# Optimization experiments

Measured on AMD Instinct MI355X. Metric: run time of the kernel, lower is better.

The kernel has to match this reference:

```python
import jax, jax.numpy as jnp
import numpy as np

B, S, D = 2, 2048, 768
H, HD = 12, 64            # num_heads, head_dim
TOPO = 128                # topology_dim
NH, HB = 8, 64            # num_hashes, hash_bits
TEMP = 0.1                # lsh_temperature
SCALE = float(np.sqrt(HD))
LSH_THRESH = 0.3
NEG = -10000.0


def setup_inputs() -> dict:
    key = jax.random.key(0)
    ks = jax.random.split(key, 12)
    hidden_states = jax.random.normal(ks[0], (B, S, D), jnp.float32)
    topo_features = jax.random.normal(ks[1], (B, S, TOPO), jnp.float32)
    attention_mask = jnp.ones((B, S), jnp.int32)
    s = 0.02
    Wq = jax.random.normal(ks[2], (D, D), jnp.float32) * s
    Wk = jax.random.normal(ks[3], (D, D), jnp.float32) * s
    Wv = jax.random.normal(ks[4], (D, D), jnp.float32) * s
    Wo = jax.random.normal(ks[5], (D, D), jnp.float32) * s
    bo = jnp.zeros((D,), jnp.float32)
    Wg = jax.random.normal(ks[6], (D + TOPO, D), jnp.float32) * s
    bg = jnp.zeros((D,), jnp.float32)
    hash_proj = jax.random.normal(ks[7], (NH, D, HB), jnp.float32) * 0.02
    topology_bias = jnp.zeros((NH, HB), jnp.float32)
    return {
        "hidden_states": hidden_states, "topo_features": topo_features,
        "Wq": Wq, "Wk": Wk, "Wv": Wv, "Wo": Wo, "bo": bo,
        "Wg": Wg, "bg": bg, "hash_proj": hash_proj,
        "topology_bias": topology_bias, "attention_mask": attention_mask,
    }


def reference(hidden_states, topo_features, Wq, Wk, Wv, Wo, bo, Wg, bg,
              hash_proj, topology_bias, attention_mask):
    hs, tf = hidden_states, topo_features
    # QKV projections -> [B,H,S,HD]
    q = (hs @ Wq).reshape(B, S, H, HD).transpose(0, 2, 1, 3)
    k = (hs @ Wk).reshape(B, S, H, HD).transpose(0, 2, 1, 3)
    v = (hs @ Wv).reshape(B, S, H, HD).transpose(0, 2, 1, 3)
    scores = jnp.einsum('bhqd,bhkd->bhqk', q, k) / SCALE  # [B,H,S,S]

    # LSH hash codes (queries == keys == hidden_states)
    proj = jnp.einsum('bsd,hdk->bshk', hs, hash_proj)
    proj = proj + TEMP * jnp.einsum('bsd,hdk->bshk', tf, hash_proj[:, :TOPO, :])
    proj = proj + topology_bias[None, None]  # [B,S,NH,HB]
    codes = jnp.sign(proj)
    # hash similarity averaged over hash tables -> [B,S,S]
    sim = jnp.einsum('bqhc,bkhc->bhqk', codes, codes) / HB
    sim = sim.mean(axis=1)
    lsh_keep = sim > LSH_THRESH
    scores = jnp.where(lsh_keep[:, None], scores, NEG)

    pad_keep = (attention_mask != 0)[:, None, None, :]  # [B,1,1,S]
    scores = jnp.where(pad_keep, scores, NEG)

    probs = jax.nn.softmax(scores, axis=-1)
    context = jnp.einsum('bhqk,bhkd->bqhd', probs, v).reshape(B, S, D)

    gate = jax.nn.sigmoid(jnp.concatenate([context, tf], axis=-1) @ Wg + bg)
    context = gate * context + (1.0 - gate) * hs
    return context @ Wo + bo
```

## Files before the change

kernel.cpp:

```cpp
#include <hip/hip_runtime.h>

typedef __attribute__((ext_vector_type(4))) float v4f;
typedef __attribute__((ext_vector_type(8))) short v8s;

#define BB 2
#define SS 2048
#define DD 768
#define HH 12
#define HDIM 64
#define NWORDS 8
#define HAM_MAX 179

#define OFF_QBF    ((size_t)0)
#define OFF_HSBF   ((size_t)31457280)
#define OFF_TFBF   ((size_t)37748736)
#define OFF_CTXBF  ((size_t)38797312)
#define OFF_CTX2BF ((size_t)45088768)
#define OFF_WTQKV  ((size_t)51380224)
#define OFF_WGT    ((size_t)54919168)
#define OFF_WOT    ((size_t)56295424)
#define OFF_HPWT   ((size_t)57475072)
#define OFF_CODES  ((size_t)66781184)
#define OFF_KEEP   ((size_t)67043328)
#define OFF_CMASK  ((size_t)68091904)

__device__ inline short f2bf(float x) {
    unsigned u = __float_as_uint(x);
    u = (u + 0x7FFFu + ((u >> 16) & 1u)) >> 16;
    return (short)u;
}
__device__ inline float bf2f(short s) {
    return __uint_as_float(((unsigned)(unsigned short)s) << 16);
}

__device__ __forceinline__ void load_lds16(const void* g, void* l) {
    __builtin_amdgcn_global_load_lds((const __attribute__((address_space(1))) void*)g,
                                     (__attribute__((address_space(3))) void*)l,
                                     16, 0, 0);
}

__global__ __launch_bounds__(256) void prep(
    const float* __restrict__ hs, const float* __restrict__ tf,
    const float* __restrict__ Wq, const float* __restrict__ Wk,
    const float* __restrict__ Wv, const float* __restrict__ Wg,
    const float* __restrict__ Wo, const float* __restrict__ hp,
    short* __restrict__ hsbf, short* __restrict__ tfbf,
    short* __restrict__ wtqkv, short* __restrict__ wgT,
    short* __restrict__ woT, short* __restrict__ hpwT,
    unsigned int* __restrict__ cmask) {
    __shared__ float T[32][33];
    const int blk = blockIdx.x;
    const int tid = threadIdx.x;
    if (blk < 1792) {
        if (blk == 0 && tid < 64) cmask[tid] = 0u;
        int i = blk * 256 + tid;
        const int na8 = 3145728 / 8;
        const float* src; short* dst; int off;
        if (i < na8) { src = hs; dst = hsbf; off = i << 3; }
        else         { src = tf; dst = tfbf; off = (i - na8) << 3; }
        float4 x = *(const float4*)(src + off);
        float4 y = *(const float4*)(src + off + 4);
        v8s r;
        r[0] = f2bf(x.x); r[1] = f2bf(x.y); r[2] = f2bf(x.z); r[3] = f2bf(x.w);
        r[4] = f2bf(y.x); r[5] = f2bf(y.y); r[6] = f2bf(y.z); r[7] = f2bf(y.w);
        *(v8s*)(dst + off) = r;
        return;
    }
    const int tx = tid & 31, ty = tid >> 5;
    if (blk < 3520) {
        int b = blk - 1792;
        int z = b / 576, rem = b % 576;
        int x = rem % 24, y = rem / 24;
        const float* W = (z == 0) ? Wq : (z == 1) ? Wk : Wv;
        short* Wt = wtqkv + (size_t)z * 589824;
        int n0 = x * 32, k0 = y * 32;
#pragma unroll
        for (int p = 0; p < 4; ++p) {
            int kk = ty + p * 8;
            T[tx][kk] = W[(size_t)(k0 + kk) * 768 + n0 + tx];
        }
        __syncthreads();
#pragma unroll
        for (int p = 0; p < 4; ++p) {
            int nn = ty + p * 8;
            Wt[(size_t)(n0 + nn) * 768 + k0 + tx] = f2bf(T[nn][tx]);
        }
    } else if (blk < 4192) {
        int b = blk - 3520;
        int x = b % 24, y = b / 24;
        int n0 = x * 32, k0 = y * 32;
#pragma unroll
        for (int p = 0; p < 4; ++p) {
            int kk = ty + p * 8;
            T[tx][kk] = Wg[(size_t)(k0 + kk) * 768 + n0 + tx];
        }
        __syncthreads();
#pragma unroll
        for (int p = 0; p < 4; ++p) {
            int nn = ty + p * 8;
            wgT[(size_t)(n0 + nn) * 896 + k0 + tx] = f2bf(T[nn][tx]);
        }
    } else if (blk < 4768) {
        int b = blk - 4192;
        int x = b % 24, y = b / 24;
        int n0 = x * 32, k0 = y * 32;
#pragma unroll
        for (int p = 0; p < 4; ++p) {
            int kk = ty + p * 8;
            T[tx][kk] = Wo[(size_t)(k0 + kk) * 768 + n0 + tx];
        }
        __syncthreads();
#pragma unroll
        for (int p = 0; p < 4; ++p) {
            int nn = ty + p * 8;
            woT[(size_t)(n0 + nn) * 768 + k0 + tx] = f2bf(T[nn][tx]);
        }
    } else {
        int b = blk - 4768;
        int x = b % 28, y = b / 28;
        int kk0 = x * 32, hc0 = y * 32;
        int h = hc0 >> 6, cb = hc0 & 63;
#pragma unroll
        for (int p = 0; p < 4; ++p) {
            int kp = ty + p * 8;
            int gk = kk0 + kp;
            int ks = (gk >= 768) ? gk - 768 : gk;
            float f = hp[((size_t)h * 768 + ks) * 64 + cb + tx];
            T[tx][kp] = (gk >= 768) ? 0.1f * f : f;
        }
        __syncthreads();
#pragma unroll
        for (int p = 0; p < 4; ++p) {
            int cp = ty + p * 8;
            hpwT[(size_t)(hc0 + cp) * 896 + kk0 + tx] = f2bf(T[cp][tx]);
        }
    }
}

template<int WN, int NW>
__global__ __launch_bounds__(256) void gemm_mfma(
    const short* __restrict__ A, const short* __restrict__ A2,
    const short* __restrict__ Bt, const short* __restrict__ Bt2,
    const float* __restrict__ bias,
    float* __restrict__ outF, short* __restrict__ outB,
    unsigned long long* __restrict__ codesOut,
    int N, int K1, int K2, int mode,
    const short* __restrict__ gctxb, const short* __restrict__ ghsb) {
    constexpr int BN = WN * 32;
    __shared__ __align__(16) short As[2 * 128 * 64];
    __shared__ __align__(16) short Bs[2 * NW * BN * 64];
    const int t = threadIdx.x;
    const int lane = t & 63, wave = t >> 6;
    const int wm = wave >> 1, wn = wave & 1;
    const int l15 = lane & 15, l4 = lane >> 4;

    const int nbx = gridDim.x;
    int flat = blockIdx.x + nbx * blockIdx.y;
    int xcd = flat & 7, j = flat >> 3;
    int by = xcd * 4 + j / nbx;
    int bx = j % nbx;
    const int row0 = by * 128;

    int nWact, col0, myMode, Kblk;
    const short* Bp;
    const float* biasp = bias;
    if (mode == 3) {
        if (bx < 12) { nWact = NW; col0 = bx * 64;        myMode = 1; Kblk = K1;      Bp = Bt;  biasp = nullptr; }
        else         { nWact = 2;  col0 = (bx - 12) * 128; myMode = 0; Kblk = K1 + K2; Bp = Bt2; }
    } else {
        nWact = 1; col0 = bx * BN; myMode = mode; Kblk = K1 + K2; Bp = Bt;
    }
    const bool sepW = (myMode == 1);

    const int lrow = lane >> 3;
    const int scolS = ((lane & 7) ^ lrow) << 3;

    auto STAGE = [&](int buf, int k0) {
        const short* Ap; int ks, strideS;
        if (k0 < K1) { Ap = A;  ks = k0;      strideS = K1; }
        else         { Ap = A2; ks = k0 - K1; strideS = K2; }
#pragma unroll
        for (int qq = 0; qq < 4; ++qq) {
            int c = wave * 4 + qq;
            const short* ga = Ap + (size_t)(row0 + c * 8 + lrow) * strideS + ks + scolS;
            load_lds16(ga, (char*)As + buf * 16384 + c * 1024);
        }
#pragma unroll
        for (int w = 0; w < NW; ++w) {
            if (w < nWact) {
#pragma unroll
                for (int qq = 0; qq < WN; ++qq) {
                    int c = wave * WN + qq;
                    size_t rowIdx = (size_t)(col0 + (sepW ? 0 : w * 64) + c * 8 + lrow);
                    const short* gb = Bp + (sepW ? (size_t)w * 589824 : (size_t)0) +
                                      rowIdx * Kblk + k0 + scolS;
                    load_lds16(gb, (char*)Bs + (buf * NW + w) * (BN * 128) + c * 1024);
                }
            }
        }
    };

    v4f acc[NW][4][WN];
#pragma unroll
    for (int w = 0; w < NW; ++w)
#pragma unroll
        for (int m = 0; m < 4; ++m)
#pragma unroll
            for (int n = 0; n < WN; ++n) acc[w][m][n] = (v4f){0.f, 0.f, 0.f, 0.f};

    const int nK = Kblk >> 6;
    STAGE(0, 0);
    __syncthreads();
    int cur = 0;
    for (int kt = 0; kt < nK; ++kt) {
        if (kt + 1 < nK) STAGE(cur ^ 1, (kt + 1) << 6);
#pragma unroll
        for (int kk = 0; kk < 2; ++kk) {
            v8s a[4];
#pragma unroll
            for (int m = 0; m < 4; ++m) {
                int row = wm * 64 + m * 16 + l15;
                int byte = (row * 128 + kk * 64 + l4 * 16) ^ ((row & 7) << 4);
                a[m] = *(const v8s*)((const char*)As + cur * 16384 + byte);
            }
#pragma unroll
            for (int w = 0; w < NW; ++w) {
                if (w < nWact) {
                    v8s b[WN];
#pragma unroll
                    for (int n = 0; n < WN; ++n) {
                        int row = wn * (WN * 16) + n * 16 + l15;
                        int byte = (row * 128 + kk * 64 + l4 * 16) ^ ((row & 7) << 4);
                        b[n] = *(const v8s*)((const char*)Bs + (cur * NW + w) * (BN * 128) + byte);
                    }
#pragma unroll
                    for (int m = 0; m < 4; ++m)
#pragma unroll
                        for (int n = 0; n < WN; ++n)
                            acc[w][m][n] = __builtin_amdgcn_mfma_f32_16x16x32_bf16(a[m], b[n], acc[w][m][n], 0, 0, 0);
                }
            }
        }
        __syncthreads();
        cur ^= 1;
    }

    if (mode == 3 && myMode == 0) {
        unsigned short* pieces = (unsigned short*)As;
#pragma unroll
        for (int w = 0; w < 2; ++w)
#pragma unroll
            for (int m = 0; m < 4; ++m)
#pragma unroll
                for (int n = 0; n < WN; ++n) {
                    int gc = col0 + w * 64 + (wn * WN + n) * 16 + l15;
                    int part = w * 4 + wn * WN + n;
#pragma unroll
                    for (int i = 0; i < 4; ++i) {
                        float c = acc[w][m][n][i] + biasp[gc];
                        unsigned long long bal = __ballot(c > 0.f);
                        if (lane < 4) {
                            int rloc = wm * 64 + m * 16 + lane * 4 + i;
                            pieces[rloc * 8 + part] = (unsigned short)(bal >> (lane * 16));
                        }
                    }
                }
        __syncthreads();
        if (t < 256) {
            int row = t >> 1, word = t & 1;
            const unsigned short* pp = pieces + row * 8 + word * 4;
            unsigned long long w64 = (unsigned long long)pp[0]
                | ((unsigned long long)pp[1] << 16)
                | ((unsigned long long)pp[2] << 32)
                | ((unsigned long long)pp[3] << 48);
            codesOut[(size_t)(row0 + row) * NWORDS + ((col0 >> 6) + word)] = w64;
        }
        return;
    }

#pragma unroll
    for (int m = 0; m < 4; ++m) {
#pragma unroll
        for (int n = 0; n < WN; ++n) {
            int gr0 = row0 + (wm * 4 + m) * 16 + l4 * 4;
            int gc = col0 + (wn * WN + n) * 16 + l15;
#pragma unroll
            for (int i = 0; i < 4; ++i) {
                int gr = gr0 + i;
                if (myMode == 1) {
                    int bb = gr >> 11, s = gr & 2047;
                    int h = gc >> 6, hd = gc & 63;
                    size_t base = (((size_t)(bb * HH + h)) * SS + s) * HDIM + hd;
#pragma unroll
                    for (int w = 0; w < NW; ++w)
                        if (w < nWact)
                            outB[(size_t)w * 3145728 + base] = f2bf(acc[w][m][n][i]);
                } else if (myMode == 0) {
                    float c = acc[0][m][n][i];
                    if (biasp) c += biasp[gc];
                    outF[(size_t)gr * N + gc] = c;
                } else {
                    float c = acc[0][m][n][i] + biasp[gc];
                    float g = 1.f / (1.f + __expf(-c));
                    size_t off = (size_t)gr * N + gc;
                    float cv = bf2f(gctxb[off]);
                    float hv = bf2f(ghsb[off]);
                    outB[off] = f2bf(g * cv + (1.f - g) * hv);
                }
            }
        }
    }
}

__global__ __launch_bounds__(256) void mask_kernel(
    const unsigned long long* __restrict__ codes, const int* __restrict__ mask,
    unsigned long long* __restrict__ keepArr, unsigned int* __restrict__ chunkmask) {
    __shared__ unsigned long long ckS[64][NWORDS];
    __shared__ int mskS[64];
    const int t = threadIdx.x;
    const int r = t >> 2, tx = t & 3;
    const int qc = blockIdx.x, kc = blockIdx.y, b = blockIdx.z;
    const int q0 = qc << 6, k0 = kc << 6;

#pragma unroll
    for (int p = 0; p < 2; ++p) {
        int idx = t + (p << 8);
        int jr = idx >> 3, ww = idx & 7;
        ckS[jr][ww ^ (jr >> 4)] =
            codes[((size_t)(b * SS + k0 + jr)) * NWORDS + ww];
    }
    if (t < 64) mskS[t] = mask[b * SS + k0 + t];
    unsigned long long cq[NWORDS];
    {
        const unsigned long long* cp = codes + ((size_t)(b * SS + q0 + r)) * NWORDS;
#pragma unroll
        for (int w = 0; w < NWORDS; ++w) cq[w] = cp[w];
    }
    __syncthreads();

    unsigned long long k64 = 0;
#pragma unroll
    for (int j16 = 0; j16 < 16; ++j16) {
        int j = (tx << 4) + j16;
        int ham = 0;
#pragma unroll
        for (int w = 0; w < NWORDS; ++w)
            ham += __popcll(cq[w] ^ ckS[j][w ^ tx]);
        if (ham <= HAM_MAX && mskS[j]) k64 |= 1ull << j;
    }
    k64 |= __shfl_xor(k64, 1, 4);
    k64 |= __shfl_xor(k64, 2, 4);
    if (tx == 0) keepArr[((size_t)(b * SS + q0 + r)) * 32 + kc] = k64;
    if (__syncthreads_or(k64 != 0) && t == 0)
        atomicOr(&chunkmask[b * 32 + qc], 1u << kc);
}

__global__ __launch_bounds__(256) void attn_kernel(
    const short* __restrict__ qm, const short* __restrict__ km,
    const short* __restrict__ vm, const unsigned long long* __restrict__ keepArr,
    const unsigned int* __restrict__ chunkmask, short* __restrict__ ctxbf) {
    __shared__ __align__(16) short Qs[64][72];
    __shared__ __align__(16) short Ks[64][72];
    __shared__ __align__(16) short VT[64][72];
    __shared__ __align__(16) short Ps[64][72];
    __shared__ unsigned long long keepS[64];
    const int t = threadIdx.x;
    const int lane = t & 63, wave = t >> 6;
    const int l15 = lane & 15, l4 = lane >> 4;
    const int q0 = blockIdx.x << 6;
    const int bh = blockIdx.y;
    const int b = bh / HH, h = bh % HH;

    {
        int r = t >> 2, seg = t & 3;
        const short* g = qm + ((size_t)bh * SS + q0 + r) * HDIM + seg * 16;
        *(int4*)&Qs[r][seg * 16] = *(const int4*)g;
        *(int4*)&Qs[r][seg * 16 + 8] = *(const int4*)(g + 8);
    }
    unsigned int cm = chunkmask[b * 32 + blockIdx.x];
    float mrun[4], lrun[4];
    v4f oacc[4];
#pragma unroll
    for (int i = 0; i < 4; ++i) { mrun[i] = -1e30f; lrun[i] = 0.f; }
#pragma unroll
    for (int n = 0; n < 4; ++n) oacc[n] = (v4f){0.f, 0.f, 0.f, 0.f};

    while (cm) {
        int kc = __ffs(cm) - 1;
        cm &= cm - 1;
        __syncthreads();
        if (t < 64) keepS[t] = keepArr[((size_t)(b * SS + q0 + t)) * 32 + kc];
        {
            int key = t >> 2, seg = t & 3;
            const short* gk = km + ((size_t)bh * SS + (kc << 6) + key) * HDIM + seg * 16;
            *(int4*)&Ks[key][seg * 16] = *(const int4*)gk;
            *(int4*)&Ks[key][seg * 16 + 8] = *(const int4*)(gk + 8);
            const short* gv = vm + ((size_t)bh * SS + (kc << 6) + key) * HDIM + seg * 16;
            int4 v0 = *(const int4*)gv, v1 = *(const int4*)(gv + 8);
            const short* s0 = (const short*)&v0;
            const short* s1 = (const short*)&v1;
#pragma unroll
            for (int e = 0; e < 8; ++e) VT[seg * 16 + e][key] = s0[e];
#pragma unroll
            for (int e = 0; e < 8; ++e) VT[seg * 16 + 8 + e][key] = s1[e];
        }
        __syncthreads();

        v8s qa0 = *(const v8s*)&Qs[wave * 16 + l15][l4 * 8];
        v8s qa1 = *(const v8s*)&Qs[wave * 16 + l15][32 + l4 * 8];
        v4f sacc[4];
#pragma unroll
        for (int n = 0; n < 4; ++n) sacc[n] = (v4f){0.f, 0.f, 0.f, 0.f};
#pragma unroll
        for (int n = 0; n < 4; ++n) {
            v8s kb0 = *(const v8s*)&Ks[n * 16 + l15][l4 * 8];
            v8s kb1 = *(const v8s*)&Ks[n * 16 + l15][32 + l4 * 8];
            sacc[n] = __builtin_amdgcn_mfma_f32_16x16x32_bf16(qa0, kb0, sacc[n], 0, 0, 0);
            sacc[n] = __builtin_amdgcn_mfma_f32_16x16x32_bf16(qa1, kb1, sacc[n], 0, 0, 0);
        }
        unsigned long long kp[4];
#pragma unroll
        for (int i = 0; i < 4; ++i) kp[i] = keepS[wave * 16 + l4 * 4 + i];
        float pe[4][4], mloc[4];
#pragma unroll
        for (int i = 0; i < 4; ++i) mloc[i] = -1e30f;
#pragma unroll
        for (int n = 0; n < 4; ++n)
#pragma unroll
            for (int i = 0; i < 4; ++i) {
                bool keep = (kp[i] >> (n * 16 + l15)) & 1;
                float sv = keep ? sacc[n][i] * 0.125f : -1e30f;
                pe[n][i] = sv;
                mloc[i] = fmaxf(mloc[i], sv);
            }
#pragma unroll
        for (int i = 0; i < 4; ++i) {
            mloc[i] = fmaxf(mloc[i], __shfl_xor(mloc[i], 1, 16));
            mloc[i] = fmaxf(mloc[i], __shfl_xor(mloc[i], 2, 16));
            mloc[i] = fmaxf(mloc[i], __shfl_xor(mloc[i], 4, 16));
            mloc[i] = fmaxf(mloc[i], __shfl_xor(mloc[i], 8, 16));
        }
        float psum[4] = {0.f, 0.f, 0.f, 0.f};
#pragma unroll
        for (int n = 0; n < 4; ++n)
#pragma unroll
            for (int i = 0; i < 4; ++i) {
                bool keep = pe[n][i] > -1e29f;
                float mnew = fmaxf(mrun[i], mloc[i]);
                float p = keep ? __expf(pe[n][i] - mnew) : 0.f;
                pe[n][i] = p;
                psum[i] += p;
            }
#pragma unroll
        for (int i = 0; i < 4; ++i) {
            psum[i] += __shfl_xor(psum[i], 1, 16);
            psum[i] += __shfl_xor(psum[i], 2, 16);
            psum[i] += __shfl_xor(psum[i], 4, 16);
            psum[i] += __shfl_xor(psum[i], 8, 16);
            float mnew = fmaxf(mrun[i], mloc[i]);
            float scale = __expf(mrun[i] - mnew);
            lrun[i] = lrun[i] * scale + psum[i];
            mrun[i] = mnew;
#pragma unroll
            for (int n = 0; n < 4; ++n) oacc[n][i] *= scale;
        }
#pragma unroll
        for (int n = 0; n < 4; ++n)
#pragma unroll
            for (int i = 0; i < 4; ++i)
                Ps[wave * 16 + l4 * 4 + i][n * 16 + l15] = f2bf(pe[n][i]);
        __syncthreads();

        v8s pa0 = *(const v8s*)&Ps[wave * 16 + l15][l4 * 8];
        v8s pa1 = *(const v8s*)&Ps[wave * 16 + l15][32 + l4 * 8];
#pragma unroll
        for (int n = 0; n < 4; ++n) {
            v8s vb0 = *(const v8s*)&VT[n * 16 + l15][l4 * 8];
            v8s vb1 = *(const v8s*)&VT[n * 16 + l15][32 + l4 * 8];
            oacc[n] = __builtin_amdgcn_mfma_f32_16x16x32_bf16(pa0, vb0, oacc[n], 0, 0, 0);
            oacc[n] = __builtin_amdgcn_mfma_f32_16x16x32_bf16(pa1, vb1, oacc[n], 0, 0, 0);
        }
    }
    float invl[4];
#pragma unroll
    for (int i = 0; i < 4; ++i) invl[i] = lrun[i] > 0.f ? 1.f / lrun[i] : 0.f;
#pragma unroll
    for (int n = 0; n < 4; ++n)
#pragma unroll
        for (int i = 0; i < 4; ++i) {
            int r = wave * 16 + l4 * 4 + i;
            size_t off = ((size_t)b * SS + q0 + r) * DD + h * HDIM + n * 16 + l15;
            ctxbf[off] = f2bf(oacc[n][i] * invl[i]);
        }
}

extern "C" void kernel_launch(void* const* d_in, const int* in_sizes, int n_in,
                              void* d_out, int out_size, void* d_ws, size_t ws_size,
                              hipStream_t stream) {
    const float* hs = (const float*)d_in[0];
    const float* tf = (const float*)d_in[1];
    const float* Wq = (const float*)d_in[2];
    const float* Wk = (const float*)d_in[3];
    const float* Wv = (const float*)d_in[4];
    const float* Wo = (const float*)d_in[5];
    const float* bo = (const float*)d_in[6];
    const float* Wg = (const float*)d_in[7];
    const float* bg = (const float*)d_in[8];
    const float* hp = (const float*)d_in[9];
    const float* tb = (const float*)d_in[10];
    const int* msk  = (const int*)d_in[11];
    float* out = (float*)d_out;

    char* w = (char*)d_ws;
    short* qkvbf  = (short*)(w + OFF_QBF);
    short* hsbf   = (short*)(w + OFF_HSBF);
    short* tfbf   = (short*)(w + OFF_TFBF);
    short* ctxbf  = (short*)(w + OFF_CTXBF);
    short* ctx2bf = (short*)(w + OFF_CTX2BF);
    short* wtqkv  = (short*)(w + OFF_WTQKV);
    short* wgT    = (short*)(w + OFF_WGT);
    short* woT    = (short*)(w + OFF_WOT);
    short* hpwT   = (short*)(w + OFF_HPWT);
    unsigned long long* codes = (unsigned long long*)(w + OFF_CODES);
    unsigned long long* keepA = (unsigned long long*)(w + OFF_KEEP);
    unsigned int* cmask = (unsigned int*)(w + OFF_CMASK);

    prep<<<dim3(5216), 256, 0, stream>>>(
        hs, tf, Wq, Wk, Wv, Wg, Wo, hp,
        hsbf, tfbf, wtqkv, wgT, woT, hpwT, cmask);
    gemm_mfma<2, 3><<<dim3(16, 32), 256, 0, stream>>>(
        hsbf, tfbf, wtqkv, hpwT, tb, nullptr, qkvbf, codes,
        512, 768, 128, 3, nullptr, nullptr);
    mask_kernel<<<dim3(32, 32, 2), 256, 0, stream>>>(codes, msk, keepA, cmask);
    attn_kernel<<<dim3(32, 24), 256, 0, stream>>>(
        qkvbf, qkvbf + 3145728, qkvbf + 2 * 3145728, keepA, cmask, ctxbf);
    gemm_mfma<2, 1><<<dim3(12, 32), 256, 0, stream>>>(
        ctxbf, tfbf, wgT, nullptr, bg, nullptr, ctx2bf, nullptr,
        768, 768, 128, 2, ctxbf, hsbf);
    gemm_mfma<2, 1><<<dim3(12, 32), 256, 0, stream>>>(
        ctx2bf, nullptr, woT, nullptr, bo, out, nullptr, nullptr,
        768, 768, 0, 0, nullptr, nullptr);
}
```

Before: 104.0 us.

## Parameterize GEMM M-tile, halve tiles for gate/output GEMMs, stage QKV stores via LDS

Adds an MF template parameter so the GEMM row-tile height (BM) is configurable. The gate and output-projection GEMMs now use 64-row tiles with twice as many blocks, to fill more compute units. Separately, the head-split QKV epilogue now stages each bf16 tile in LDS and writes it out as contiguous 16-byte vector stores instead of scattered 2-byte stores. Smaller tiles give less reuse per block, and the staging adds extra barriers.

```diff
diff --git a/kernel.cpp b/kernel.cpp
--- a/kernel.cpp
+++ b/kernel.cpp
@@ -137,7 +137,7 @@
     }
 }
 
-template<int WN, int NW>
+template<int WN, int NW, int MF>
 __global__ __launch_bounds__(256) void gemm_mfma(
     const short* __restrict__ A, const short* __restrict__ A2,
     const short* __restrict__ Bt, const short* __restrict__ Bt2,
@@ -147,7 +147,8 @@
     int N, int K1, int K2, int mode,
     const short* __restrict__ gctxb, const short* __restrict__ ghsb) {
     constexpr int BN = WN * 32;
-    __shared__ __align__(16) short As[2 * 128 * 64];
+    constexpr int BM = MF * 32;
+    __shared__ __align__(16) short As[2 * BM * 64];
     __shared__ __align__(16) short Bs[2 * NW * BN * 64];
     const int t = threadIdx.x;
     const int lane = t & 63, wave = t >> 6;
@@ -155,17 +156,18 @@
     const int l15 = lane & 15, l4 = lane >> 4;
 
     const int nbx = gridDim.x;
+    const int perXcd = gridDim.y >> 3;
     int flat = blockIdx.x + nbx * blockIdx.y;
     int xcd = flat & 7, j = flat >> 3;
-    int by = xcd * 4 + j / nbx;
+    int by = xcd * perXcd + j / nbx;
     int bx = j % nbx;
-    const int row0 = by * 128;
+    const int row0 = by * BM;
 
     int nWact, col0, myMode, Kblk;
     const short* Bp;
     const float* biasp = bias;
     if (mode == 3) {
-        if (bx < 12) { nWact = NW; col0 = bx * 64;        myMode = 1; Kblk = K1;      Bp = Bt;  biasp = nullptr; }
+        if (bx < 12) { nWact = NW; col0 = bx * 64;         myMode = 1; Kblk = K1;      Bp = Bt;  biasp = nullptr; }
         else         { nWact = 2;  col0 = (bx - 12) * 128; myMode = 0; Kblk = K1 + K2; Bp = Bt2; }
     } else {
         nWact = 1; col0 = bx * BN; myMode = mode; Kblk = K1 + K2; Bp = Bt;
@@ -180,10 +182,10 @@
         if (k0 < K1) { Ap = A;  ks = k0;      strideS = K1; }
         else         { Ap = A2; ks = k0 - K1; strideS = K2; }
 #pragma unroll
-        for (int qq = 0; qq < 4; ++qq) {
-            int c = wave * 4 + qq;
+        for (int qq = 0; qq < MF; ++qq) {
+            int c = wave * MF + qq;
             const short* ga = Ap + (size_t)(row0 + c * 8 + lrow) * strideS + ks + scolS;
-            load_lds16(ga, (char*)As + buf * 16384 + c * 1024);
+            load_lds16(ga, (char*)As + buf * (BM * 128) + c * 1024);
         }
 #pragma unroll
         for (int w = 0; w < NW; ++w) {
@@ -200,11 +202,11 @@
         }
     };
 
-    v4f acc[NW][4][WN];
+    v4f acc[NW][MF][WN];
 #pragma unroll
     for (int w = 0; w < NW; ++w)
 #pragma unroll
-        for (int m = 0; m < 4; ++m)
+        for (int m = 0; m < MF; ++m)
 #pragma unroll
             for (int n = 0; n < WN; ++n) acc[w][m][n] = (v4f){0.f, 0.f, 0.f, 0.f};
 
@@ -216,12 +218,12 @@
         if (kt + 1 < nK) STAGE(cur ^ 1, (kt + 1) << 6);
 #pragma unroll
         for (int kk = 0; kk < 2; ++kk) {
-            v8s a[4];
-#pragma unroll
-            for (int m = 0; m < 4; ++m) {
-                int row = wm * 64 + m * 16 + l15;
+            v8s a[MF];
+#pragma unroll
+            for (int m = 0; m < MF; ++m) {
+                int row = wm * (MF * 16) + m * 16 + l15;
                 int byte = (row * 128 + kk * 64 + l4 * 16) ^ ((row & 7) << 4);
-                a[m] = *(const v8s*)((const char*)As + cur * 16384 + byte);
+                a[m] = *(const v8s*)((const char*)As + cur * (BM * 128) + byte);
             }
 #pragma unroll
             for (int w = 0; w < NW; ++w) {
@@ -234,7 +236,7 @@
                         b[n] = *(const v8s*)((const char*)Bs + (cur * NW + w) * (BN * 128) + byte);
                     }
 #pragma unroll
-                    for (int m = 0; m < 4; ++m)
+                    for (int m = 0; m < MF; ++m)
 #pragma unroll
                         for (int n = 0; n < WN; ++n)
                             acc[w][m][n] = __builtin_amdgcn_mfma_f32_16x16x32_bf16(a[m], b[n], acc[w][m][n], 0, 0, 0);
@@ -250,7 +252,7 @@
 #pragma unroll
         for (int w = 0; w < 2; ++w)
 #pragma unroll
-            for (int m = 0; m < 4; ++m)
+            for (int m = 0; m < MF; ++m)
 #pragma unroll
                 for (int n = 0; n < WN; ++n) {
                     int gc = col0 + w * 64 + (wn * WN + n) * 16 + l15;
@@ -260,7 +262,7 @@
                         float c = acc[w][m][n][i] + biasp[gc];
                         unsigned long long bal = __ballot(c > 0.f);
                         if (lane < 4) {
-                            int rloc = wm * 64 + m * 16 + lane * 4 + i;
+                            int rloc = wm * (MF * 16) + m * 16 + lane * 4 + i;
                             pieces[rloc * 8 + part] = (unsigned short)(bal >> (lane * 16));
                         }
                     }
@@ -278,24 +280,48 @@
         return;
     }
 
-#pragma unroll
-    for (int m = 0; m < 4; ++m) {
+    if (myMode == 1) {
+        short* stg = (short*)As;
+        const int hh = col0 >> 6;
+        const int bb = row0 >> 11;
+        const int s0 = row0 & 2047;
+#pragma unroll
+        for (int w = 0; w < NW; ++w) {
+            if (w < nWact) {
+                __syncthreads();
+#pragma unroll
+                for (int m = 0; m < MF; ++m)
+#pragma unroll
+                    for (int n = 0; n < WN; ++n) {
+                        int r = wm * (MF * 16) + m * 16 + l4 * 4;
+                        int c = (wn * WN + n) * 16 + l15;
+#pragma unroll
+                        for (int i = 0; i < 4; ++i)
+                            stg[(r + i) * 64 + c] = f2bf(acc[w][m][n][i]);
+                    }
+                __syncthreads();
+                short* dst = outB + (size_t)w * 3145728 +
+                             (((size_t)(bb * HH + hh)) * SS + s0) * HDIM;
+                const char* src = (const char*)stg + t * (BM / 2);
+                char* d = (char*)dst + t * (BM / 2);
+#pragma unroll
+                for (int q = 0; q < BM / 32; ++q)
+                    *(int4*)(d + q * 16) = *(const int4*)(src + q * 16);
+            }
+        }
+        return;
+    }
+
+#pragma unroll
+    for (int m = 0; m < MF; ++m) {
 #pragma unroll
         for (int n = 0; n < WN; ++n) {
-            int gr0 = row0 + (wm * 4 + m) * 16 + l4 * 4;
+            int gr0 = row0 + (wm * MF + m) * 16 + l4 * 4;
             int gc = col0 + (wn * WN + n) * 16 + l15;
 #pragma unroll
             for (int i = 0; i < 4; ++i) {
                 int gr = gr0 + i;
-                if (myMode == 1) {
-                    int bb = gr >> 11, s = gr & 2047;
-                    int h = gc >> 6, hd = gc & 63;
-                    size_t base = (((size_t)(bb * HH + h)) * SS + s) * HDIM + hd;
-#pragma unroll
-                    for (int w = 0; w < NW; ++w)
-                        if (w < nWact)
-                            outB[(size_t)w * 3145728 + base] = f2bf(acc[w][m][n][i]);
-                } else if (myMode == 0) {
+                if (myMode == 0) {
                     float c = acc[0][m][n][i];
                     if (biasp) c += biasp[gc];
                     outF[(size_t)gr * N + gc] = c;
@@ -528,16 +554,16 @@
     prep<<<dim3(5216), 256, 0, stream>>>(
         hs, tf, Wq, Wk, Wv, Wg, Wo, hp,
         hsbf, tfbf, wtqkv, wgT, woT, hpwT, cmask);
-    gemm_mfma<2, 3><<<dim3(16, 32), 256, 0, stream>>>(
+    gemm_mfma<2, 3, 4><<<dim3(16, 32), 256, 0, stream>>>(
         hsbf, tfbf, wtqkv, hpwT, tb, nullptr, qkvbf, codes,
         512, 768, 128, 3, nullptr, nullptr);
     mask_kernel<<<dim3(32, 32, 2), 256, 0, stream>>>(codes, msk, keepA, cmask);
     attn_kernel<<<dim3(32, 24), 256, 0, stream>>>(
         qkvbf, qkvbf + 3145728, qkvbf + 2 * 3145728, keepA, cmask, ctxbf);
-    gemm_mfma<2, 1><<<dim3(12, 32), 256, 0, stream>>>(
+    gemm_mfma<2, 1, 2><<<dim3(12, 64), 256, 0, stream>>>(
         ctxbf, tfbf, wgT, nullptr, bg, nullptr, ctx2bf, nullptr,
         768, 768, 128, 2, ctxbf, hsbf);
-    gemm_mfma<2, 1><<<dim3(12, 32), 256, 0, stream>>>(
+    gemm_mfma<2, 1, 2><<<dim3(12, 64), 256, 0, stream>>>(
         ctx2bf, nullptr, woT, nullptr, bo, out, nullptr, nullptr,
         768, 768, 0, 0, nullptr, nullptr);
 }
```

Result: faster. 94.45 us (-9.2%).
